# Performance work log

Measured on AMD Instinct MI355X. Metric: run time of the kernel, lower is better.

## Reference

```python
import jax, jax.numpy as jnp
import numpy as np

K = 10      # neighbors; conv width math 10 -> 3 -> 1
EPS = 1e-5  # InstanceNorm2d default eps (affine=False)
NEG = 0.2   # leaky relu slope


def _instnorm(x):
    m = x.mean(axis=(2, 3), keepdims=True)
    v = x.var(axis=(2, 3), keepdims=True)  # biased var, as in torch instance_norm
    return (x - m) * jax.lax.rsqrt(v + EPS)


def _conv13(x, w, b, s):
    y = jax.lax.conv_general_dilated(x, w, (1, s), 'VALID',
                                     dimension_numbers=('NCHW', 'OIHW', 'NCHW'))
    return y + b[None, :, None, None]


def _block(x, wA, bA, wB, bB):
    # Sequential(conv(1,3,stride(1,3)), IN, ReLU, conv(1,3), IN, ReLU)
    y = jax.nn.relu(_instnorm(_conv13(x, wA, bA, 3)))
    return jax.nn.relu(_instnorm(_conv13(y, wB, bB, 1)))


def _knn_idx(coords, k):
    # coords [B,2,N] -> k nearest neighbor indices [B,N,k] (self excluded)
    pts = coords.transpose(0, 2, 1)
    sq = (pts ** 2).sum(-1)
    dist = sq[:, :, None] + sq[:, None, :] - 2.0 * jnp.einsum('bnc,bmc->bnm', pts, pts)
    dist = jnp.clip(dist, 1e-12)
    _, idx = jax.lax.top_k(-dist, k + 1)  # smallest distances, sorted
    return idx[:, :, 1:]


def _gather_nb(x, idx):
    # x [B,C,N], idx [B,N,k] -> [B,C,N,k]
    return jax.vmap(lambda f, i: f[:, i])(x, idx)


def _graph_feat(feats, idx):
    nb = _gather_nb(feats, idx)
    ctr = jnp.broadcast_to(feats[..., None], nb.shape)
    return jnp.concatenate([ctr, nb - ctr], axis=1)  # [B,2C,N,k]


def _cos_angle(coords, idx):
    nei = _gather_nb(coords, idx)          # [B,2,N,k]
    ctr = coords[..., None]                # [B,2,N,1]
    dot = (ctr * nei).sum(axis=1, keepdims=True)
    na = jnp.sqrt((ctr ** 2).sum(axis=1, keepdims=True))
    nb = jnp.sqrt((nei ** 2).sum(axis=1, keepdims=True))
    return dot / (na * nb)                 # [B,1,N,k]


def _c1(w, x):
    # 1x1 conv, no bias
    return jnp.einsum('oi,bihw->bohw', w, x)


def _forward(coords, features, W1, W2, W3, W3o, a1wA, a1bA, a1wB, a1bB,
             a2wA, a2bA, a2wB, a2bB, angwA, angbA, angwB, angbB):
    B, C, N = features.shape
    lrelu = lambda x: jax.nn.leaky_relu(x, NEG)
    x0 = features[..., None]
    # KNN depends only on coords: all three torch graph builds give identical indices
    idx = _knn_idx(coords, K)
    x1_old = _graph_feat(features, idx)                         # [B,2C,N,K]
    x1 = _block(x1_old, a1wA, a1bA, a1wB, a1bB)                 # [B,C,N,1]
    # angle_enc1 is shared and idx identical -> f_ang1 == f_ang2
    f_ang = _block(_cos_angle(coords, idx), angwA, angbA, angwB, angbB)
    x2 = _block(_graph_feat(x1[..., 0], idx), a2wA, a2bA, a2wB, a2bB)
    x3 = jnp.concatenate([x0, x1 + f_ang, x2 + f_ang], axis=1)  # [B,3C,N,1]
    x3 = lrelu(_instnorm(_c1(W3, x3))).reshape(B, -1, N)
    x1o = lrelu(_instnorm(_c1(W1, x1_old))).max(axis=-1, keepdims=True)   # [B,C,N,1]
    x2o = lrelu(_instnorm(_c1(W2, _graph_feat(x1o[..., 0], idx)))).max(axis=-1, keepdims=True)
    x3o = jnp.concatenate([x0, x1o, x2o], axis=1)               # [B,4C,N,1]
    x3o = lrelu(_instnorm(_c1(W3o, x3o))).reshape(B, -1, N)
    return x3 + x3o


def setup_inputs():
    key = jax.random.key(0)
    ks = jax.random.split(key, 20)
    B, C, N = 4, 128, 4096
    r = lambda i, shp, sc=1.0: jax.random.normal(ks[i], shp, jnp.float32) * sc
    s = 0.05
    return {
        'coords': r(0, (B, 2, N)),
        'features': r(1, (B, C, N)),
        'W1': r(2, (C, 2 * C), s),
        'W2': r(3, (2 * C, 2 * C), s),
        'W3': r(4, (C, 3 * C), s),
        'W3o': r(5, (C, 4 * C), s),
        'a1wA': r(6, (C, 2 * C, 1, 3), s), 'a1bA': r(7, (C,), s),
        'a1wB': r(8, (C, C, 1, 3), s), 'a1bB': r(9, (C,), s),
        'a2wA': r(10, (C, 2 * C, 1, 3), s), 'a2bA': r(11, (C,), s),
        'a2wB': r(12, (C, C, 1, 3), s), 'a2bB': r(13, (C,), s),
        'angwA': r(14, (C, 1, 1, 3), s), 'angbA': r(15, (C,), s),
        'angwB': r(16, (C, C, 1, 3), s), 'angbB': r(17, (C,), s),
    }


def reference(coords, features, W1, W2, W3, W3o, a1wA, a1bA, a1wB, a1bB,
              a2wA, a2bA, a2wB, a2bB, angwA, angbA, angwB, angbB):
    return _forward(coords, features, W1, W2, W3, W3o, a1wA, a1bA, a1wB, a1bB,
                    a2wA, a2bA, a2wB, a2bB, angwA, angbA, angwB, angbB)
```

## Files before the change

### kernel.cpp

```cpp
#include <hip/hip_runtime.h>
#include <hip/hip_bf16.h>

typedef unsigned long long ull;

#define BN 4
#define CH 128
#define NP 4096
#define KNB 10
#define EPSI 1e-5f
#define GM_PTS 16
#define CA_PTS 16

#define FMA4(A, W, F) do { (A).x += (W).x*(F); (A).y += (W).y*(F); \
                           (A).z += (W).z*(F); (A).w += (W).w*(F); } while(0)

__device__ __forceinline__ ull shfl_xor_u64(ull v, int mask) {
    unsigned lo = (unsigned)(v & 0xFFFFFFFFu);
    unsigned hi = (unsigned)(v >> 32);
    lo = __shfl_xor(lo, mask);
    hi = __shfl_xor(hi, mask);
    return ((ull)hi << 32) | lo;
}

__device__ __forceinline__ int clampj(int j) { return ((unsigned)j < (unsigned)NP) ? j : 0; }

__device__ __forceinline__ unsigned short f2bf(float f) {
    unsigned u = __float_as_uint(f);
    unsigned r = u + 0x7FFFu + ((u >> 16) & 1u);
    return (unsigned short)(r >> 16);
}
__device__ __forceinline__ float bf2f(unsigned short h) {
    return __uint_as_float(((unsigned)h) << 16);
}
__device__ __forceinline__ float4 bfload4(const unsigned short* p) {
    ushort4 h = *(const ushort4*)p;
    float4 r; r.x = bf2f(h.x); r.y = bf2f(h.y); r.z = bf2f(h.z); r.w = bf2f(h.w);
    return r;
}

__device__ __forceinline__ void d_packA(const float* w, float* WT, int i) {
    int co = i % CH, ci = (i / CH) % CH, s = i / (CH * CH);
    float val;
    if (s == 0) {
        val = 0.f;
        for (int dk = 0; dk < 3; dk++)
            val += w[(co * 256 + ci) * 3 + dk] - w[(co * 256 + 128 + ci) * 3 + dk];
    } else {
        val = w[(co * 256 + 128 + ci) * 3 + (s - 1)];
    }
    WT[i] = val;
}
__device__ __forceinline__ void d_packB(const float* w, float* WT, int i) {
    int co = i % CH, ci = (i / CH) % CH, dk = i / (CH * CH);
    WT[i] = w[(co * CH + ci) * 3 + dk];
}
__device__ __forceinline__ void d_packUV(const float* w, float* Wu, float* Wn, int Cout, int i) {
    int co = i % Cout, ci = i / Cout;
    float a = w[co * 256 + ci], bb = w[co * 256 + 128 + ci];
    Wu[i] = a - bb; Wn[i] = bb;
}
__device__ __forceinline__ void d_packP(const float* w, float* WT, int Cin, int Cout, int i) {
    int co = i % Cout, ci = i / Cout;
    WT[i] = w[co * Cin + ci];
}

__global__ void pack_all(const float* __restrict__ a1wA, const float* __restrict__ a2wA,
                         const float* __restrict__ a1wB, const float* __restrict__ a2wB,
                         const float* __restrict__ angwB, const float* __restrict__ W1,
                         const float* __restrict__ W2, const float* __restrict__ W3,
                         const float* __restrict__ W3o, const float* __restrict__ angwA,
                         float* __restrict__ WA1T, float* __restrict__ WA2T,
                         float* __restrict__ WB1T, float* __restrict__ WB2T,
                         float* __restrict__ WBAT,
                         float* __restrict__ W1U, float* __restrict__ W1N,
                         float* __restrict__ W2U, float* __restrict__ W2N,
                         float* __restrict__ W3T, float* __restrict__ W3OT,
                         float* __restrict__ WANGA) {
    int i = blockIdx.x * 256 + threadIdx.x;
    const int sA = 4 * CH * CH;
    const int sB = 3 * CH * CH;
    if (i < sA) { d_packA(a1wA, WA1T, i); return; } i -= sA;
    if (i < sA) { d_packA(a2wA, WA2T, i); return; } i -= sA;
    if (i < sB) { d_packB(a1wB, WB1T, i); return; } i -= sB;
    if (i < sB) { d_packB(a2wB, WB2T, i); return; } i -= sB;
    if (i < sB) { d_packB(angwB, WBAT, i); return; } i -= sB;
    if (i < CH * CH) { d_packUV(W1, W1U, W1N, CH, i); return; } i -= CH * CH;
    if (i < CH * 256) { d_packUV(W2, W2U, W2N, 256, i); return; } i -= CH * 256;
    if (i < 384 * CH) { d_packP(W3, W3T, 384, CH, i); return; } i -= 384 * CH;
    if (i < 512 * CH) { d_packP(W3o, W3OT, 512, CH, i); return; } i -= 512 * CH;
    if (i < 3 * CH) { d_packP(angwA, WANGA, 3, CH, i); return; }
}

__global__ void ftrans_kernel(const float* __restrict__ feats, float* __restrict__ F) {
    int i = blockIdx.x * 256 + threadIdx.x;
    if (i >= BN * CH * NP) return;
    int n = i % NP, c = (i / NP) % CH, b = i / (NP * CH);
    F[(b * NP + n) * CH + c] = feats[i];
}

__global__ void knn_kernel(const float* __restrict__ coords, int* __restrict__ IDX) {
    int gw = blockIdx.x * 4 + (threadIdx.x >> 6);
    int b = gw / NP;
    int n = gw % NP;
    int lane = threadIdx.x & 63;
    float xn = coords[(b * 2 + 0) * NP + n];
    float yn = coords[(b * 2 + 1) * NP + n];
    float sn = __fadd_rn(__fmul_rn(xn, xn), __fmul_rn(yn, yn));
    ull a[11];
    #pragma unroll
    for (int q = 0; q < 11; q++) a[q] = 0xFFFFFFFFFFFFFFFFULL;
    for (int m = lane; m < NP; m += 64) {
        float xm = coords[(b * 2 + 0) * NP + m];
        float ym = coords[(b * 2 + 1) * NP + m];
        float sm = __fadd_rn(__fmul_rn(xm, xm), __fmul_rn(ym, ym));
        float dot = __fmaf_rn(yn, ym, __fmul_rn(xn, xm));
        float d = __fsub_rn(__fadd_rn(sn, sm), __fmul_rn(2.0f, dot));
        d = fmaxf(d, 1e-12f);
        ull key = ((ull)__float_as_uint(d) << 32) | (unsigned)m;
        if (key < a[10]) {
            a[10] = key;
            #pragma unroll
            for (int q = 10; q > 0; --q)
                if (a[q] < a[q - 1]) { ull t = a[q]; a[q] = a[q - 1]; a[q - 1] = t; }
        }
    }
    for (int r = 0; r < 11; ++r) {
        ull k = a[0];
        ull mk = k;
        #pragma unroll
        for (int off = 1; off < 64; off <<= 1) {
            ull o = shfl_xor_u64(mk, off);
            mk = (o < mk) ? o : mk;
        }
        if (k == mk) {
            #pragma unroll
            for (int q = 0; q < 10; ++q) a[q] = a[q + 1];
            a[10] = 0xFFFFFFFFFFFFFFFFULL;
        }
        if (lane == 0 && r > 0) IDX[(b * NP + n) * KNB + (r - 1)] = (int)(mk & 0xFFFFFFFFu);
    }
}

__global__ void cosangle_kernel(const float* __restrict__ coords, const int* __restrict__ IDX,
                                float* __restrict__ COSA) {
    int i = blockIdx.x * 256 + threadIdx.x;
    if (i >= BN * NP * KNB) return;
    int n = (i / KNB) % NP, b = i / (KNB * NP);
    int j = clampj(IDX[i]);
    float xc = coords[(b * 2 + 0) * NP + n], yc = coords[(b * 2 + 1) * NP + n];
    float xm = coords[(b * 2 + 0) * NP + j], ym = coords[(b * 2 + 1) * NP + j];
    float dot = xc * xm + yc * ym;
    float na = sqrtf(xc * xc + yc * yc);
    float nb2 = sqrtf(xm * xm + ym * ym);
    COSA[i] = dot / fmaxf(na * nb2, 1e-30f);
}

__global__ __launch_bounds__(256) void convA_kernel(const float* __restrict__ Fin,
                             const int* __restrict__ IDX,
                             const float* __restrict__ WT, float* __restrict__ YA,
                             float* __restrict__ PART,
                             const float* __restrict__ STATS, int slot) {
    __shared__ __align__(16) float ctr[CA_PTS][CH];
    __shared__ __align__(16) unsigned short nbh[CA_PTS][9][CH];
    __shared__ int jidx[CA_PTS * 9];
    int b = blockIdx.x / (NP / CA_PTS);
    int chunk = blockIdx.x % (NP / CA_PTS);
    int n0 = chunk * CA_PTS;
    int cog = threadIdx.x & 31;
    int pg  = threadIdx.x >> 5;
    const float* SB = (slot >= 0) ? &STATS[((size_t)(slot * BN + b) * 256) * 2] : nullptr;
    if (threadIdx.x < CA_PTS * 9) {
        int n = threadIdx.x / 9, kk = threadIdx.x % 9;
        jidx[threadIdx.x] = clampj(IDX[(b * NP + n0 + n) * KNB + kk]);
    }
    __syncthreads();
    for (int v4 = threadIdx.x; v4 < CA_PTS * 32; v4 += 256) {
        int n = v4 >> 5, c4 = v4 & 31;
        float4 x = *(const float4*)&Fin[(size_t)(b * NP + n0 + n) * CH + c4 * 4];
        if (SB) {
            float4 s0 = *(const float4*)&SB[c4 * 8];
            float4 s1 = *(const float4*)&SB[c4 * 8 + 4];
            x.x = fmaxf((x.x - s0.x) * s0.y, 0.f);
            x.y = fmaxf((x.y - s0.z) * s0.w, 0.f);
            x.z = fmaxf((x.z - s1.x) * s1.y, 0.f);
            x.w = fmaxf((x.w - s1.z) * s1.w, 0.f);
        }
        *(float4*)&ctr[n][c4 * 4] = x;
    }
    for (int v4 = threadIdx.x; v4 < CA_PTS * 9 * 32; v4 += 256) {
        int n = v4 / 288, rem = v4 % 288, kk = rem >> 5, c4 = rem & 31;
        float4 x = *(const float4*)&Fin[(size_t)(b * NP + jidx[n * 9 + kk]) * CH + c4 * 4];
        if (SB) {
            float4 s0 = *(const float4*)&SB[c4 * 8];
            float4 s1 = *(const float4*)&SB[c4 * 8 + 4];
            x.x = fmaxf((x.x - s0.x) * s0.y, 0.f);
            x.y = fmaxf((x.y - s0.z) * s0.w, 0.f);
            x.z = fmaxf((x.z - s1.x) * s1.y, 0.f);
            x.w = fmaxf((x.w - s1.z) * s1.w, 0.f);
        }
        ushort4 h;
        h.x = f2bf(x.x); h.y = f2bf(x.y); h.z = f2bf(x.z); h.w = f2bf(x.w);
        *(ushort4*)&nbh[n][kk][c4 * 4] = h;
    }
    __syncthreads();
    const float4* W4 = (const float4*)WT;
    const int p0 = pg * 2, p1 = pg * 2 + 1;
    float4 cacc0, cacc1;
    cacc0.x = cacc0.y = cacc0.z = cacc0.w = 0.f;
    cacc1 = cacc0;
    for (int ci = 0; ci < CH; ci += 4) {
        float4 xa = *(const float4*)&ctr[p0][ci];
        float4 xb = *(const float4*)&ctr[p1][ci];
        #pragma unroll
        for (int u = 0; u < 4; ++u) {
            float4 w = W4[(ci + u) * 32 + cog];
            float fa = ((const float*)&xa)[u];
            float fb = ((const float*)&xb)[u];
            FMA4(cacc0, w, fa); FMA4(cacc1, w, fb);
        }
    }
    float4 t00 = cacc0, t01 = cacc0, t02 = cacc0;
    float4 t10 = cacc1, t11 = cacc1, t12 = cacc1;
    for (int dk = 0; dk < 3; ++dk) {
        const float4* Wd = W4 + (size_t)(1 + dk) * (CH * 32);
        const unsigned short* a00 = &nbh[p0][0 * 3 + dk][0];
        const unsigned short* a01 = &nbh[p0][1 * 3 + dk][0];
        const unsigned short* a02 = &nbh[p0][2 * 3 + dk][0];
        const unsigned short* a10 = &nbh[p1][0 * 3 + dk][0];
        const unsigned short* a11 = &nbh[p1][1 * 3 + dk][0];
        const unsigned short* a12 = &nbh[p1][2 * 3 + dk][0];
        for (int ci = 0; ci < CH; ci += 4) {
            float4 x00 = bfload4(&a00[ci]);
            float4 x01 = bfload4(&a01[ci]);
            float4 x02 = bfload4(&a02[ci]);
            float4 x10 = bfload4(&a10[ci]);
            float4 x11 = bfload4(&a11[ci]);
            float4 x12 = bfload4(&a12[ci]);
            #pragma unroll
            for (int u = 0; u < 4; ++u) {
                float4 w = Wd[(ci + u) * 32 + cog];
                FMA4(t00, w, ((const float*)&x00)[u]);
                FMA4(t01, w, ((const float*)&x01)[u]);
                FMA4(t02, w, ((const float*)&x02)[u]);
                FMA4(t10, w, ((const float*)&x10)[u]);
                FMA4(t11, w, ((const float*)&x11)[u]);
                FMA4(t12, w, ((const float*)&x12)[u]);
            }
        }
    }
    {
        size_t base0 = ((size_t)(b * NP + n0 + p0) * 3) * CH + cog * 4;
        *(float4*)&YA[base0 + 0 * CH] = t00;
        *(float4*)&YA[base0 + 1 * CH] = t01;
        *(float4*)&YA[base0 + 2 * CH] = t02;
        size_t base1 = ((size_t)(b * NP + n0 + p1) * 3) * CH + cog * 4;
        *(float4*)&YA[base1 + 0 * CH] = t10;
        *(float4*)&YA[base1 + 1 * CH] = t11;
        *(float4*)&YA[base1 + 2 * CH] = t12;
    }
    float s4[4], q4[4];
    s4[0] = t00.x + t01.x + t02.x + t10.x + t11.x + t12.x;
    s4[1] = t00.y + t01.y + t02.y + t10.y + t11.y + t12.y;
    s4[2] = t00.z + t01.z + t02.z + t10.z + t11.z + t12.z;
    s4[3] = t00.w + t01.w + t02.w + t10.w + t11.w + t12.w;
    q4[0] = t00.x*t00.x + t01.x*t01.x + t02.x*t02.x + t10.x*t10.x + t11.x*t11.x + t12.x*t12.x;
    q4[1] = t00.y*t00.y + t01.y*t01.y + t02.y*t02.y + t10.y*t10.y + t11.y*t11.y + t12.y*t12.y;
    q4[2] = t00.z*t00.z + t01.z*t01.z + t02.z*t02.z + t10.z*t10.z + t11.z*t11.z + t12.z*t12.z;
    q4[3] = t00.w*t00.w + t01.w*t01.w + t02.w*t02.w + t10.w*t10.w + t11.w*t11.w + t12.w*t12.w;
    __syncthreads();
    float* red = (float*)&nbh[0][0][0];
    #pragma unroll
    for (int j = 0; j < 4; ++j) {
        red[((pg * 32 + cog) * 4 + j) * 2 + 0] = s4[j];
        red[((pg * 32 + cog) * 4 + j) * 2 + 1] = q4[j];
    }
    __syncthreads();
    if (threadIdx.x < CH) {
        int c = threadIdx.x;
        float ss = 0.f, qq = 0.f;
        #pragma unroll
        for (int g = 0; g < 8; ++g) {
            ss += red[((g * 32 + (c >> 2)) * 4 + (c & 3)) * 2 + 0];
            qq += red[((g * 32 + (c >> 2)) * 4 + (c & 3)) * 2 + 1];
        }
        PART[((size_t)(b * (NP / CA_PTS) + chunk) * 256 + c) * 2 + 0] = ss;
        PART[((size_t)(b * (NP / CA_PTS) + chunk) * 256 + c) * 2 + 1] = qq;
    }
}

__global__ void angA_kernel(const float* __restrict__ COSA, const float* __restrict__ WT,
                            float* __restrict__ YA, float* __restrict__ PART) {
    __shared__ float ca[32][10];
    int b = blockIdx.x / (NP / 32);
    int chunk = blockIdx.x % (NP / 32);
    int n0 = chunk * 32;
    int co = threadIdx.x;
    for (int v = threadIdx.x; v < 320; v += 128) {
        int nn = v / 10, kk = v % 10;
        ca[nn][kk] = COSA[(b * NP + n0 + nn) * KNB + kk];
    }
    float w0 = WT[co], w1 = WT[CH + co], w2 = WT[2 * CH + co];
    __syncthreads();
    float sum = 0.f, sq = 0.f;
    for (int nn = 0; nn < 32; nn++) {
        #pragma unroll
        for (int t = 0; t < 3; t++) {
            float v = w0 * ca[nn][3 * t] + w1 * ca[nn][3 * t + 1] + w2 * ca[nn][3 * t + 2];
            YA[((b * NP + n0 + nn) * 3 + t) * CH + co] = v;
            sum += v; sq += v * v;
        }
    }
    PART[((b * (NP / 32) + chunk) * 256 + co) * 2 + 0] = sum;
    PART[((b * (NP / 32) + chunk) * 256 + co) * 2 + 1] = sq;
}

template <int CIN, int NCOG>
__device__ __forceinline__ void gemm_16pt(const float* lds, const float* __restrict__ WT,
                                          int cog, int pg, float4 acc[4]) {
    const float4* W4 = (const float4*)WT;
    const float* xb = lds + pg * 4 * CIN;
    for (int ci = 0; ci < CIN; ci += 4) {
        float4 x0 = *(const float4*)&xb[0 * CIN + ci];
        float4 x1 = *(const float4*)&xb[1 * CIN + ci];
        float4 x2 = *(const float4*)&xb[2 * CIN + ci];
        float4 x3 = *(const float4*)&xb[3 * CIN + ci];
        #pragma unroll
        for (int u = 0; u < 4; ++u) {
            float4 w = W4[(ci + u) * NCOG + cog];
            float f0 = ((const float*)&x0)[u];
            float f1 = ((const float*)&x1)[u];
            float f2 = ((const float*)&x2)[u];
            float f3 = ((const float*)&x3)[u];
            FMA4(acc[0], w, f0); FMA4(acc[1], w, f1);
            FMA4(acc[2], w, f2); FMA4(acc[3], w, f3);
        }
    }
}

template <int NCOG>
__device__ __forceinline__ void reduce_stats(const float* s4, const float* q4,
                                             float* red, float* __restrict__ PART,
                                             int b, int chunk, int nchunks,
                                             int pg, int cog) {
    constexpr int COUT = NCOG * 4;
    __syncthreads();
    #pragma unroll
    for (int j = 0; j < 4; ++j) {
        red[((pg * NCOG + cog) * 4 + j) * 2 + 0] = s4[j];
        red[((pg * NCOG + cog) * 4 + j) * 2 + 1] = q4[j];
    }
    __syncthreads();
    int c = threadIdx.x;
    if (c < COUT) {
        float ss = 0.f, qq = 0.f;
        #pragma unroll
        for (int g = 0; g < 4; ++g) {
            ss += red[((g * NCOG + (c >> 2)) * 4 + (c & 3)) * 2 + 0];
            qq += red[((g * NCOG + (c >> 2)) * 4 + (c & 3)) * 2 + 1];
        }
        PART[((size_t)(b * nchunks + chunk) * 256 + c) * 2 + 0] = ss;
        PART[((size_t)(b * nchunks + chunk) * 256 + c) * 2 + 1] = qq;
    }
}

template <int NCOG>
__device__ __forceinline__ void out16(const float4 acc[4], float* __restrict__ OUT,
                                      int b, int n0, int pg, int cog,
                                      float s4[4], float q4[4]) {
    constexpr int COUT = NCOG * 4;
    #pragma unroll
    for (int p = 0; p < 4; ++p) {
        *(float4*)&OUT[(size_t)(b * NP + n0 + pg * 4 + p) * COUT + cog * 4] = acc[p];
        s4[0] += acc[p].x; s4[1] += acc[p].y; s4[2] += acc[p].z; s4[3] += acc[p].w;
        q4[0] += acc[p].x * acc[p].x; q4[1] += acc[p].y * acc[p].y;
        q4[2] += acc[p].z * acc[p].z; q4[3] += acc[p].w * acc[p].w;
    }
}

template <int CIN, int NCOG>
__global__ void pixel_gemm_t(const float* __restrict__ IN_, const float* __restrict__ WT,
                             float* __restrict__ OUT, const float* __restrict__ STATS,
                             int slot, int act, float* __restrict__ PART) {
    constexpr int COUT = NCOG * 4;
    constexpr int BD = 4 * NCOG;
    __shared__ __align__(16) float ldsin[16 * CIN];
    int b = blockIdx.x / (NP / 16);
    int chunk = blockIdx.x % (NP / 16);
    int n0 = chunk * 16;
    int cog = threadIdx.x & (NCOG - 1);
    int pg = threadIdx.x / NCOG;
    constexpr int nv4 = 16 * CIN / 4;
    if (slot >= 0) {
        int cbase = (4 * threadIdx.x) & 127;
        const float* st = &STATS[((slot * BN + b) * 256 + cbase) * 2];
        float m0 = st[0], r0 = st[1], m1 = st[2], r1 = st[3];
        float m2 = st[4], r2 = st[5], m3 = st[6], r3 = st[7];
        for (int v4 = threadIdx.x; v4 < nv4; v4 += BD) {
            float4 x = *(const float4*)&IN_[(size_t)(b * NP + n0) * CIN + 4 * v4];
            float v0 = (x.x - m0) * r0, v1 = (x.y - m1) * r1;
            float v2 = (x.z - m2) * r2, v3 = (x.w - m3) * r3;
            if (act) {
                x.x = (v0 >= 0.f) ? v0 : 0.2f * v0;
                x.y = (v1 >= 0.f) ? v1 : 0.2f * v1;
                x.z = (v2 >= 0.f) ? v2 : 0.2f * v2;
                x.w = (v3 >= 0.f) ? v3 : 0.2f * v3;
            } else {
                x.x = fmaxf(v0, 0.f); x.y = fmaxf(v1, 0.f);
                x.z = fmaxf(v2, 0.f); x.w = fmaxf(v3, 0.f);
            }
            *(float4*)&ldsin[4 * v4] = x;
        }
    } else {
        for (int v4 = threadIdx.x; v4 < nv4; v4 += BD)
            *(float4*)&ldsin[4 * v4] =
                *(const float4*)&IN_[(size_t)(b * NP + n0) * CIN + 4 * v4];
    }
    __syncthreads();
    float4 acc[4];
    #pragma unroll
    for (int p = 0; p < 4; ++p) acc[p].x = acc[p].y = acc[p].z = acc[p].w = 0.f;
    gemm_16pt<CIN, NCOG>(ldsin, WT, cog, pg, acc);
    float s4[4] = {0,0,0,0}, q4[4] = {0,0,0,0};
    out16<NCOG>(acc, OUT, b, n0, pg, cog, s4, q4);
    if (PART)
        reduce_stats<NCOG>(s4, q4, ldsin, PART, b, chunk, NP / 16, pg, cog);
}

__global__ void stats_final(const float* __restrict__ PART, float* __restrict__ STATS,
                            int S, int Cc, int slot, int nch) {
    __shared__ float ssum[256], ssq[256];
    int bc = blockIdx.x;
    int b = bc / Cc, c = bc % Cc;
    float sum = 0.f, sq = 0.f;
    for (int ch = threadIdx.x; ch < nch; ch += 256) {
        sum += PART[((b * nch + ch) * 256 + c) * 2 + 0];
        sq  += PART[((b * nch + ch) * 256 + c) * 2 + 1];
    }
    ssum[threadIdx.x] = sum; ssq[threadIdx.x] = sq;
    __syncthreads();
    for (int s = 128; s > 0; s >>= 1) {
        if (threadIdx.x < s) {
            ssum[threadIdx.x] += ssum[threadIdx.x + s];
            ssq[threadIdx.x]  += ssq[threadIdx.x + s];
        }
        __syncthreads();
    }
    if (threadIdx.x == 0) {
        float mean = ssum[0] / (float)S;
        float var = fmaxf(ssq[0] / (float)S - mean * mean, 0.f);
        STATS[((slot * BN + b) * 256 + c) * 2 + 0] = mean;
        STATS[((slot * BN + b) * 256 + c) * 2 + 1] = rsqrtf(var + EPSI);
    }
}

template <int NCOG>
__global__ void gathermax_t(const float* __restrict__ X, const float* __restrict__ Wu,
                            const float* __restrict__ V, const int* __restrict__ IDX,
                            float* __restrict__ M, float* __restrict__ PART,
                            const float* __restrict__ STATS, int slot) {
    constexpr int COUT = NCOG * 4;
    __shared__ __align__(16) float rows[GM_PTS * CH];
    int b = blockIdx.x / (NP / GM_PTS);
    int chunk = blockIdx.x % (NP / GM_PTS);
    int n0 = chunk * GM_PTS;
    int cog = threadIdx.x & (NCOG - 1);
    int pg = threadIdx.x / NCOG;
    if (slot >= 0) {
        int c0 = (4 * threadIdx.x) & 127;
        const float* st = &STATS[((slot * BN + b) * 256 + c0) * 2];
        float m0 = st[0], r0 = st[1], m1 = st[2], r1 = st[3];
        float m2 = st[4], r2 = st[5], m3 = st[6], r3 = st[7];
        for (int v4 = threadIdx.x; v4 < GM_PTS * CH / 4; v4 += COUT) {
            float4 x = *(const float4*)&X[(size_t)(b * NP + n0) * CH + v4 * 4];
            float v0 = (x.x - m0) * r0, v1 = (x.y - m1) * r1;
            float v2 = (x.z - m2) * r2, v3 = (x.w - m3) * r3;
            x.x = (v0 >= 0.f) ? v0 : 0.2f * v0;
            x.y = (v1 >= 0.f) ? v1 : 0.2f * v1;
            x.z = (v2 >= 0.f) ? v2 : 0.2f * v2;
            x.w = (v3 >= 0.f) ? v3 : 0.2f * v3;
            *(float4*)&rows[v4 * 4] = x;
        }
    } else {
        for (int v4 = threadIdx.x; v4 < GM_PTS * CH / 4; v4 += COUT)
            *(float4*)&rows[v4 * 4] = *(const float4*)&X[(size_t)(b * NP + n0) * CH + v4 * 4];
    }
    __syncthreads();
    float4 acc[4];
    #pragma unroll
    for (int p = 0; p < 4; ++p) acc[p].x = acc[p].y = acc[p].z = acc[p].w = 0.f;
    gemm_16pt<CH, NCOG>(rows, Wu, cog, pg, acc);
    float s4[4] = {0,0,0,0}, q4[4] = {0,0,0,0};
    #pragma unroll
    for (int p = 0; p < 4; ++p) {
        int nn = n0 + pg * 4 + p;
        float4 u = acc[p];
        float4 best; best.x = best.y = best.z = best.w = -3.4e38f;
        for (int k = 0; k < KNB; ++k) {
            int j = clampj(IDX[(b * NP + nn) * KNB + k]);
            float4 vv = *(const float4*)&V[(size_t)(b * NP + j) * COUT + cog * 4];
            vv.x += u.x; vv.y += u.y; vv.z += u.z; vv.w += u.w;
            s4[0] += vv.x; s4[1] += vv.y; s4[2] += vv.z; s4[3] += vv.w;
            q4[0] += vv.x * vv.x; q4[1] += vv.y * vv.y;
            q4[2] += vv.z * vv.z; q4[3] += vv.w * vv.w;
            best.x = fmaxf(best.x, vv.x); best.y = fmaxf(best.y, vv.y);
            best.z = fmaxf(best.z, vv.z); best.w = fmaxf(best.w, vv.w);
        }
        *(float4*)&M[(size_t)(b * NP + nn) * COUT + cog * 4] = best;
    }
    __syncthreads();
    reduce_stats<NCOG>(s4, q4, rows, PART, b, chunk, NP / GM_PTS, pg, cog);
}

__global__ void head3_kernel(const float* __restrict__ F, const float* __restrict__ X1,
                             const float* __restrict__ X2, const float* __restrict__ FANG,
                             const float* __restrict__ WT, float* __restrict__ Y3,
                             float* __restrict__ PART, const float* __restrict__ STATS) {
    __shared__ __align__(16) float lds[16 * 384];
    int b = blockIdx.x / (NP / 16);
    int chunk = blockIdx.x % (NP / 16);
    int n0 = chunk * 16;
    int cog = threadIdx.x & 31;
    int pg = threadIdx.x >> 5;
    const float* S1 = &STATS[((size_t)(1 * BN + b) * 256) * 2];
    const float* S5 = &STATS[((size_t)(5 * BN + b) * 256) * 2];
    const float* S3 = &STATS[((size_t)(3 * BN + b) * 256) * 2];
    for (int v4 = threadIdx.x; v4 < 16 * 96; v4 += 128) {
        int nn = v4 / 96, q4 = v4 % 96;
        int part = q4 >> 5, c4 = q4 & 31;
        size_t base = (size_t)(b * NP + n0 + nn) * CH + c4 * 4;
        float4 val;
        if (part == 0) val = *(const float4*)&F[base];
        else {
            const float* src = (part == 1) ? X1 : X2;
            const float* SX = (part == 1) ? S1 : S5;
            float4 xx = *(const float4*)&src[base];
            float4 aa = *(const float4*)&FANG[base];
            float4 sx0 = *(const float4*)&SX[c4 * 8];
            float4 sx1 = *(const float4*)&SX[c4 * 8 + 4];
            float4 sa0 = *(const float4*)&S3[c4 * 8];
            float4 sa1 = *(const float4*)&S3[c4 * 8 + 4];
            val.x = fmaxf((xx.x - sx0.x) * sx0.y, 0.f) + fmaxf((aa.x - sa0.x) * sa0.y, 0.f);
            val.y = fmaxf((xx.y - sx0.z) * sx0.w, 0.f) + fmaxf((aa.y - sa0.z) * sa0.w, 0.f);
            val.z = fmaxf((xx.z - sx1.x) * sx1.y, 0.f) + fmaxf((aa.z - sa1.x) * sa1.y, 0.f);
            val.w = fmaxf((xx.w - sx1.z) * sx1.w, 0.f) + fmaxf((aa.w - sa1.z) * sa1.w, 0.f);
        }
        *(float4*)&lds[v4 * 4] = val;
    }
    __syncthreads();
    float4 acc[4];
    #pragma unroll
    for (int p = 0; p < 4; ++p) acc[p].x = acc[p].y = acc[p].z = acc[p].w = 0.f;
    gemm_16pt<384, 32>(lds, WT, cog, pg, acc);
    float s4[4] = {0,0,0,0}, q4[4] = {0,0,0,0};
    out16<32>(acc, Y3, b, n0, pg, cog, s4, q4);
    reduce_stats<32>(s4, q4, lds, PART, b, chunk, NP / 16, pg, cog);
}

__global__ void head3o_kernel(const float* __restrict__ F, const float* __restrict__ X1O,
                              const float* __restrict__ X2O, const float* __restrict__ WT,
                              float* __restrict__ Y3O, float* __restrict__ PART,
                              const float* __restrict__ STATS) {
    __shared__ __align__(16) float lds[16 * 512];
    int b = blockIdx.x / (NP / 16);
    int chunk = blockIdx.x % (NP / 16);
    int n0 = chunk * 16;
    int cog = threadIdx.x & 31;
    int pg = threadIdx.x >> 5;
    const float* S6 = &STATS[((size_t)(6 * BN + b) * 256) * 2];
    const float* S7 = &STATS[((size_t)(7 * BN + b) * 256) * 2];
    for (int v4 = threadIdx.x; v4 < 16 * 128; v4 += 128) {
        int nn = v4 >> 7, q4 = v4 & 127;
        float4 val;
        if (q4 < 32) {
            val = *(const float4*)&F[(size_t)(b * NP + n0 + nn) * CH + q4 * 4];
        } else if (q4 < 64) {
            int c4 = q4 - 32;
            float4 x = *(const float4*)&X1O[(size_t)(b * NP + n0 + nn) * CH + c4 * 4];
            float4 s0 = *(const float4*)&S6[c4 * 8];
            float4 s1 = *(const float4*)&S6[c4 * 8 + 4];
            float v0 = (x.x - s0.x) * s0.y, v1 = (x.y - s0.z) * s0.w;
            float v2 = (x.z - s1.x) * s1.y, v3 = (x.w - s1.z) * s1.w;
            val.x = (v0 >= 0.f) ? v0 : 0.2f * v0;
            val.y = (v1 >= 0.f) ? v1 : 0.2f * v1;
            val.z = (v2 >= 0.f) ? v2 : 0.2f * v2;
            val.w = (v3 >= 0.f) ? v3 : 0.2f * v3;
        } else {
            int c4 = q4 - 64;
            float4 x = *(const float4*)&X2O[(size_t)(b * NP + n0 + nn) * 256 + c4 * 4];
            float4 s0 = *(const float4*)&S7[c4 * 8];
            float4 s1 = *(const float4*)&S7[c4 * 8 + 4];
            float v0 = (x.x - s0.x) * s0.y, v1 = (x.y - s0.z) * s0.w;
            float v2 = (x.z - s1.x) * s1.y, v3 = (x.w - s1.z) * s1.w;
            val.x = (v0 >= 0.f) ? v0 : 0.2f * v0;
            val.y = (v1 >= 0.f) ? v1 : 0.2f * v1;
            val.z = (v2 >= 0.f) ? v2 : 0.2f * v2;
            val.w = (v3 >= 0.f) ? v3 : 0.2f * v3;
        }
        *(float4*)&lds[v4 * 4] = val;
    }
    __syncthreads();
    float4 acc[4];
    #pragma unroll
    for (int p = 0; p < 4; ++p) acc[p].x = acc[p].y = acc[p].z = acc[p].w = 0.f;
    gemm_16pt<512, 32>(lds, WT, cog, pg, acc);
    float s4[4] = {0,0,0,0}, q4[4] = {0,0,0,0};
    out16<32>(acc, Y3O, b, n0, pg, cog, s4, q4);
    reduce_stats<32>(s4, q4, lds, PART, b, chunk, NP / 16, pg, cog);
}

__global__ void final_kernel(const float* __restrict__ Y3, const float* __restrict__ Y3O,
                             const float* __restrict__ STATS, float* __restrict__ out) {
    __shared__ float T[64][129];
    int b = blockIdx.x / (NP / 64);
    int n0 = (blockIdx.x % (NP / 64)) * 64;
    int co = threadIdx.x;
    float m3 = STATS[((8 * BN + b) * 256 + co) * 2 + 0];
    float r3 = STATS[((8 * BN + b) * 256 + co) * 2 + 1];
    float m3o = STATS[((9 * BN + b) * 256 + co) * 2 + 0];
    float r3o = STATS[((9 * BN + b) * 256 + co) * 2 + 1];
    for (int j = 0; j < 64; j++) {
        size_t idx = (size_t)(b * NP + n0 + j) * CH + co;
        float v3 = (Y3[idx] - m3) * r3;
        v3 = (v3 >= 0.f) ? v3 : 0.2f * v3;
        float v3o = (Y3O[idx] - m3o) * r3o;
        v3o = (v3o >= 0.f) ? v3o : 0.2f * v3o;
        T[j][co] = v3 + v3o;
    }
    __syncthreads();
    for (int rr = 0; rr < 64; rr++) {
        int r = rr * 2 + (threadIdx.x >> 6);
        int j = threadIdx.x & 63;
        out[(size_t)(b * CH + r) * NP + n0 + j] = T[j][r];
    }
}

extern "C" void kernel_launch(void* const* d_in, const int* in_sizes, int n_in,
                              void* d_out, int out_size, void* d_ws, size_t ws_size,
                              hipStream_t stream) {
    const float* coords   = (const float*)d_in[0];
    const float* features = (const float*)d_in[1];
    const float* W1   = (const float*)d_in[2];
    const float* W2   = (const float*)d_in[3];
    const float* W3   = (const float*)d_in[4];
    const float* W3o  = (const float*)d_in[5];
    const float* a1wA = (const float*)d_in[6];
    const float* a1wB = (const float*)d_in[8];
    const float* a2wA = (const float*)d_in[10];
    const float* a2wB = (const float*)d_in[12];
    const float* angwA = (const float*)d_in[14];
    const float* angwB = (const float*)d_in[16];
    float* out = (float*)d_out;
    float* ws = (float*)d_ws;
    (void)ws_size; (void)in_sizes; (void)n_in; (void)out_size;

    size_t off = 0;
    float* WA1T  = ws + off; off += 4 * CH * CH;
    float* WA2T  = ws + off; off += 4 * CH * CH;
    float* WB1T  = ws + off; off += 3 * CH * CH;
    float* WB2T  = ws + off; off += 3 * CH * CH;
    float* WBAT  = ws + off; off += 3 * CH * CH;
    float* WANGA = ws + off; off += 512;
    float* W1U   = ws + off; off += CH * CH;
    float* W1N   = ws + off; off += CH * CH;
    float* W2U   = ws + off; off += CH * 256;
    float* W2N   = ws + off; off += CH * 256;
    float* W3T   = ws + off; off += 384 * CH;
    float* W3OT  = ws + off; off += 512 * CH;
    int*   IDX   = (int*)(ws + off); off += (size_t)BN * NP * KNB;
    float* COSA  = ws + off; off += (size_t)BN * NP * KNB;
    float* PART  = ws + off; off += (size_t)BN * 1024 * 256 * 2;
    float* STATS = ws + off; off += 10 * BN * 256 * 2;
    const size_t UNIT = (size_t)BN * NP * CH;
    float* POOL  = ws + off; off += 7 * UNIT;

    float* F    = POOL + 0 * UNIT;
    float* YA   = POOL + 1 * UNIT;
    float* X1   = POOL + 4 * UNIT;
    float* FANG = POOL + 5 * UNIT;
    float* X2   = POOL + 6 * UNIT;
    float* Y3   = POOL + 1 * UNIT;
    float* V1   = POOL + 2 * UNIT;
    float* M1   = POOL + 6 * UNIT;
    float* V2   = POOL + 4 * UNIT;
    float* M2   = POOL + 2 * UNIT;
    float* Y3O  = POOL + 4 * UNIT;

    pack_all<<<1730, 256, 0, stream>>>(a1wA, a2wA, a1wB, a2wB, angwB, W1, W2, W3, W3o, angwA,
                                       WA1T, WA2T, WB1T, WB2T, WBAT,
                                       W1U, W1N, W2U, W2N, W3T, W3OT, WANGA);

    ftrans_kernel<<<(BN * CH * NP + 255) / 256, 256, 0, stream>>>(features, F);
    knn_kernel<<<BN * NP / 4, 256, 0, stream>>>(coords, IDX);
    cosangle_kernel<<<(BN * NP * KNB + 255) / 256, 256, 0, stream>>>(coords, IDX, COSA);

    auto sfin = [&](int S, int Cc, int slot, int nch) {
        stats_final<<<BN * Cc, 256, 0, stream>>>(PART, STATS, S, Cc, slot, nch);
    };

    convA_kernel<<<BN * (NP / CA_PTS), 256, 0, stream>>>(F, IDX, WA1T, YA, PART, STATS, -1);
    sfin(3 * NP, CH, 0, NP / CA_PTS);
    pixel_gemm_t<384, 32><<<BN * (NP / 16), 128, 0, stream>>>(YA, WB1T, X1, STATS, 0, 0, PART);
    sfin(NP, CH, 1, NP / 16);

    angA_kernel<<<BN * (NP / 32), 128, 0, stream>>>(COSA, WANGA, YA, PART);
    sfin(3 * NP, CH, 2, NP / 32);
    pixel_gemm_t<384, 32><<<BN * (NP / 16), 128, 0, stream>>>(YA, WBAT, FANG, STATS, 2, 0, PART);
    sfin(NP, CH, 3, NP / 16);

    convA_kernel<<<BN * (NP / CA_PTS), 256, 0, stream>>>(X1, IDX, WA2T, YA, PART, STATS, 1);
    sfin(3 * NP, CH, 4, NP / CA_PTS);
    pixel_gemm_t<384, 32><<<BN * (NP / 16), 128, 0, stream>>>(YA, WB2T, X2, STATS, 4, 0, PART);
    sfin(NP, CH, 5, NP / 16);

    head3_kernel<<<BN * (NP / 16), 128, 0, stream>>>(F, X1, X2, FANG, W3T, Y3, PART, STATS);
    sfin(NP, CH, 8, NP / 16);

    pixel_gemm_t<128, 32><<<BN * (NP / 16), 128, 0, stream>>>(F, W1N, V1, STATS, -1, 0, nullptr);
    gathermax_t<32><<<BN * (NP / GM_PTS), 128, 0, stream>>>(F, W1U, V1, IDX, M1, PART, STATS, -1);
    sfin(NP * KNB, CH, 6, NP / GM_PTS);

    pixel_gemm_t<128, 64><<<BN * (NP / 16), 256, 0, stream>>>(M1, W2N, V2, STATS, 6, 1, nullptr);
    gathermax_t<64><<<BN * (NP / GM_PTS), 256, 0, stream>>>(M1, W2U, V2, IDX, M2, PART, STATS, 6);
    sfin(NP * KNB, 256, 7, NP / GM_PTS);

    head3o_kernel<<<BN * (NP / 16), 128, 0, stream>>>(F, M1, M2, W3OT, Y3O, PART, STATS);
    sfin(NP, CH, 9, NP / 16);
    final_kernel<<<BN * (NP / 64), 128, 0, stream>>>(Y3, Y3O, STATS, out);
}
```

Measured before the change: 841.7 us.

## Double points per block in pixel GEMMs and stage inputs as bf16 in LDS

The per-point GEMM kernels (pixel_gemm_t, head3, head3o) now process 32 points per block instead of 16, with each thread holding 8 point accumulators. Each weight float4 loaded from global memory is therefore reused across twice as many points. Inputs are staged in shared memory as bf16, which keeps the LDS footprint the same and halves LDS read traffic. The trade-offs are bf16 rounding of activations, which costs accuracy, more registers per thread, and half as many blocks. The stats partial counts are updated to match.

```diff
diff --git a/kernel.cpp b/kernel.cpp
--- a/kernel.cpp
+++ b/kernel.cpp
@@ -36,6 +36,10 @@
     ushort4 h = *(const ushort4*)p;
     float4 r; r.x = bf2f(h.x); r.y = bf2f(h.y); r.z = bf2f(h.z); r.w = bf2f(h.w);
     return r;
+}
+__device__ __forceinline__ ushort4 bf4(float4 x) {
+    ushort4 h; h.x = f2bf(x.x); h.y = f2bf(x.y); h.z = f2bf(x.z); h.w = f2bf(x.w);
+    return h;
 }
 
 __device__ __forceinline__ void d_packA(const float* w, float* WT, int i) {
@@ -198,9 +202,7 @@
             x.z = fmaxf((x.z - s1.x) * s1.y, 0.f);
             x.w = fmaxf((x.w - s1.z) * s1.w, 0.f);
         }
-        ushort4 h;
-        h.x = f2bf(x.x); h.y = f2bf(x.y); h.z = f2bf(x.z); h.w = f2bf(x.w);
-        *(ushort4*)&nbh[n][kk][c4 * 4] = h;
+        *(ushort4*)&nbh[n][kk][c4 * 4] = bf4(x);
     }
     __syncthreads();
     const float4* W4 = (const float4*)WT;
@@ -337,6 +339,36 @@
     }
 }
 
+template <int CIN, int NCOG>
+__device__ __forceinline__ void gemm_32pt(const unsigned short* lds,
+                                          const float* __restrict__ WT,
+                                          int cog, int pg, float4 acc[8]) {
+    const float4* W4 = (const float4*)WT;
+    const unsigned short* xb = lds + pg * 8 * CIN;
+    for (int ci = 0; ci < CIN; ci += 4) {
+        float4 x0 = bfload4(&xb[0 * CIN + ci]);
+        float4 x1 = bfload4(&xb[1 * CIN + ci]);
+        float4 x2 = bfload4(&xb[2 * CIN + ci]);
+        float4 x3 = bfload4(&xb[3 * CIN + ci]);
+        float4 x4 = bfload4(&xb[4 * CIN + ci]);
+        float4 x5 = bfload4(&xb[5 * CIN + ci]);
+        float4 x6 = bfload4(&xb[6 * CIN + ci]);
+        float4 x7 = bfload4(&xb[7 * CIN + ci]);
+        #pragma unroll
+        for (int u = 0; u < 4; ++u) {
+            float4 w = W4[(ci + u) * NCOG + cog];
+            FMA4(acc[0], w, ((const float*)&x0)[u]);
+            FMA4(acc[1], w, ((const float*)&x1)[u]);
+            FMA4(acc[2], w, ((const float*)&x2)[u]);
+            FMA4(acc[3], w, ((const float*)&x3)[u]);
+            FMA4(acc[4], w, ((const float*)&x4)[u]);
+            FMA4(acc[5], w, ((const float*)&x5)[u]);
+            FMA4(acc[6], w, ((const float*)&x6)[u]);
+            FMA4(acc[7], w, ((const float*)&x7)[u]);
+        }
+    }
+}
+
 template <int NCOG>
 __device__ __forceinline__ void reduce_stats(const float* s4, const float* q4,
                                              float* red, float* __restrict__ PART,
@@ -364,13 +396,13 @@
 }
 
 template <int NCOG>
-__device__ __forceinline__ void out16(const float4 acc[4], float* __restrict__ OUT,
+__device__ __forceinline__ void out32(const float4 acc[8], float* __restrict__ OUT,
                                       int b, int n0, int pg, int cog,
                                       float s4[4], float q4[4]) {
     constexpr int COUT = NCOG * 4;
     #pragma unroll
-    for (int p = 0; p < 4; ++p) {
-        *(float4*)&OUT[(size_t)(b * NP + n0 + pg * 4 + p) * COUT + cog * 4] = acc[p];
+    for (int p = 0; p < 8; ++p) {
+        *(float4*)&OUT[(size_t)(b * NP + n0 + pg * 8 + p) * COUT + cog * 4] = acc[p];
         s4[0] += acc[p].x; s4[1] += acc[p].y; s4[2] += acc[p].z; s4[3] += acc[p].w;
         q4[0] += acc[p].x * acc[p].x; q4[1] += acc[p].y * acc[p].y;
         q4[2] += acc[p].z * acc[p].z; q4[3] += acc[p].w * acc[p].w;
@@ -383,13 +415,13 @@
                              int slot, int act, float* __restrict__ PART) {
     constexpr int COUT = NCOG * 4;
     constexpr int BD = 4 * NCOG;
-    __shared__ __align__(16) float ldsin[16 * CIN];
-    int b = blockIdx.x / (NP / 16);
-    int chunk = blockIdx.x % (NP / 16);
-    int n0 = chunk * 16;
+    __shared__ __align__(16) unsigned short ldsin[32 * CIN];
+    int b = blockIdx.x / (NP / 32);
+    int chunk = blockIdx.x % (NP / 32);
+    int n0 = chunk * 32;
     int cog = threadIdx.x & (NCOG - 1);
     int pg = threadIdx.x / NCOG;
-    constexpr int nv4 = 16 * CIN / 4;
+    constexpr int nv4 = 32 * CIN / 4;
     if (slot >= 0) {
         int cbase = (4 * threadIdx.x) & 127;
         const float* st = &STATS[((slot * BN + b) * 256 + cbase) * 2];
@@ -408,22 +440,23 @@
                 x.x = fmaxf(v0, 0.f); x.y = fmaxf(v1, 0.f);
                 x.z = fmaxf(v2, 0.f); x.w = fmaxf(v3, 0.f);
             }
-            *(float4*)&ldsin[4 * v4] = x;
+            *(ushort4*)&ldsin[4 * v4] = bf4(x);
         }
     } else {
-        for (int v4 = threadIdx.x; v4 < nv4; v4 += BD)
-            *(float4*)&ldsin[4 * v4] =
-                *(const float4*)&IN_[(size_t)(b * NP + n0) * CIN + 4 * v4];
-    }
-    __syncthreads();
-    float4 acc[4];
-    #pragma unroll
-    for (int p = 0; p < 4; ++p) acc[p].x = acc[p].y = acc[p].z = acc[p].w = 0.f;
-    gemm_16pt<CIN, NCOG>(ldsin, WT, cog, pg, acc);
+        for (int v4 = threadIdx.x; v4 < nv4; v4 += BD) {
+            float4 x = *(const float4*)&IN_[(size_t)(b * NP + n0) * CIN + 4 * v4];
+            *(ushort4*)&ldsin[4 * v4] = bf4(x);
+        }
+    }
+    __syncthreads();
+    float4 acc[8];
+    #pragma unroll
+    for (int p = 0; p < 8; ++p) acc[p].x = acc[p].y = acc[p].z = acc[p].w = 0.f;
+    gemm_32pt<CIN, NCOG>(ldsin, WT, cog, pg, acc);
     float s4[4] = {0,0,0,0}, q4[4] = {0,0,0,0};
-    out16<NCOG>(acc, OUT, b, n0, pg, cog, s4, q4);
+    out32<NCOG>(acc, OUT, b, n0, pg, cog, s4, q4);
     if (PART)
-        reduce_stats<NCOG>(s4, q4, ldsin, PART, b, chunk, NP / 16, pg, cog);
+        reduce_stats<NCOG>(s4, q4, (float*)ldsin, PART, b, chunk, NP / 32, pg, cog);
 }
 
 __global__ void stats_final(const float* __restrict__ PART, float* __restrict__ STATS,
@@ -515,16 +548,16 @@
                              const float* __restrict__ X2, const float* __restrict__ FANG,
                              const float* __restrict__ WT, float* __restrict__ Y3,
                              float* __restrict__ PART, const float* __restrict__ STATS) {
-    __shared__ __align__(16) float lds[16 * 384];
-    int b = blockIdx.x / (NP / 16);
-    int chunk = blockIdx.x % (NP / 16);
-    int n0 = chunk * 16;
+    __shared__ __align__(16) unsigned short lds[32 * 384];
+    int b = blockIdx.x / (NP / 32);
+    int chunk = blockIdx.x % (NP / 32);
+    int n0 = chunk * 32;
     int cog = threadIdx.x & 31;
     int pg = threadIdx.x >> 5;
     const float* S1 = &STATS[((size_t)(1 * BN + b) * 256) * 2];
     const float* S5 = &STATS[((size_t)(5 * BN + b) * 256) * 2];
     const float* S3 = &STATS[((size_t)(3 * BN + b) * 256) * 2];
-    for (int v4 = threadIdx.x; v4 < 16 * 96; v4 += 128) {
+    for (int v4 = threadIdx.x; v4 < 32 * 96; v4 += 128) {
         int nn = v4 / 96, q4 = v4 % 96;
         int part = q4 >> 5, c4 = q4 & 31;
         size_t base = (size_t)(b * NP + n0 + nn) * CH + c4 * 4;
@@ -544,31 +577,31 @@
             val.z = fmaxf((xx.z - sx1.x) * sx1.y, 0.f) + fmaxf((aa.z - sa1.x) * sa1.y, 0.f);
             val.w = fmaxf((xx.w - sx1.z) * sx1.w, 0.f) + fmaxf((aa.w - sa1.z) * sa1.w, 0.f);
         }
-        *(float4*)&lds[v4 * 4] = val;
-    }
-    __syncthreads();
-    float4 acc[4];
-    #pragma unroll
-    for (int p = 0; p < 4; ++p) acc[p].x = acc[p].y = acc[p].z = acc[p].w = 0.f;
-    gemm_16pt<384, 32>(lds, WT, cog, pg, acc);
+        *(ushort4*)&lds[v4 * 4] = bf4(val);
+    }
+    __syncthreads();
+    float4 acc[8];
+    #pragma unroll
+    for (int p = 0; p < 8; ++p) acc[p].x = acc[p].y = acc[p].z = acc[p].w = 0.f;
+    gemm_32pt<384, 32>(lds, WT, cog, pg, acc);
     float s4[4] = {0,0,0,0}, q4[4] = {0,0,0,0};
-    out16<32>(acc, Y3, b, n0, pg, cog, s4, q4);
-    reduce_stats<32>(s4, q4, lds, PART, b, chunk, NP / 16, pg, cog);
+    out32<32>(acc, Y3, b, n0, pg, cog, s4, q4);
+    reduce_stats<32>(s4, q4, (float*)lds, PART, b, chunk, NP / 32, pg, cog);
 }
 
 __global__ void head3o_kernel(const float* __restrict__ F, const float* __restrict__ X1O,
                               const float* __restrict__ X2O, const float* __restrict__ WT,
                               float* __restrict__ Y3O, float* __restrict__ PART,
                               const float* __restrict__ STATS) {
-    __shared__ __align__(16) float lds[16 * 512];
-    int b = blockIdx.x / (NP / 16);
-    int chunk = blockIdx.x % (NP / 16);
-    int n0 = chunk * 16;
+    __shared__ __align__(16) unsigned short lds[32 * 512];
+    int b = blockIdx.x / (NP / 32);
+    int chunk = blockIdx.x % (NP / 32);
+    int n0 = chunk * 32;
     int cog = threadIdx.x & 31;
     int pg = threadIdx.x >> 5;
     const float* S6 = &STATS[((size_t)(6 * BN + b) * 256) * 2];
     const float* S7 = &STATS[((size_t)(7 * BN + b) * 256) * 2];
-    for (int v4 = threadIdx.x; v4 < 16 * 128; v4 += 128) {
+    for (int v4 = threadIdx.x; v4 < 32 * 128; v4 += 128) {
         int nn = v4 >> 7, q4 = v4 & 127;
         float4 val;
         if (q4 < 32) {
@@ -596,16 +629,16 @@
             val.z = (v2 >= 0.f) ? v2 : 0.2f * v2;
             val.w = (v3 >= 0.f) ? v3 : 0.2f * v3;
         }
-        *(float4*)&lds[v4 * 4] = val;
-    }
-    __syncthreads();
-    float4 acc[4];
-    #pragma unroll
-    for (int p = 0; p < 4; ++p) acc[p].x = acc[p].y = acc[p].z = acc[p].w = 0.f;
-    gemm_16pt<512, 32>(lds, WT, cog, pg, acc);
+        *(ushort4*)&lds[v4 * 4] = bf4(val);
+    }
+    __syncthreads();
+    float4 acc[8];
+    #pragma unroll
+    for (int p = 0; p < 8; ++p) acc[p].x = acc[p].y = acc[p].z = acc[p].w = 0.f;
+    gemm_32pt<512, 32>(lds, WT, cog, pg, acc);
     float s4[4] = {0,0,0,0}, q4[4] = {0,0,0,0};
-    out16<32>(acc, Y3O, b, n0, pg, cog, s4, q4);
-    reduce_stats<32>(s4, q4, lds, PART, b, chunk, NP / 16, pg, cog);
+    out32<32>(acc, Y3O, b, n0, pg, cog, s4, q4);
+    reduce_stats<32>(s4, q4, (float*)lds, PART, b, chunk, NP / 32, pg, cog);
 }
 
 __global__ void final_kernel(const float* __restrict__ Y3, const float* __restrict__ Y3O,
@@ -699,31 +732,31 @@
 
     convA_kernel<<<BN * (NP / CA_PTS), 256, 0, stream>>>(F, IDX, WA1T, YA, PART, STATS, -1);
     sfin(3 * NP, CH, 0, NP / CA_PTS);
-    pixel_gemm_t<384, 32><<<BN * (NP / 16), 128, 0, stream>>>(YA, WB1T, X1, STATS, 0, 0, PART);
-    sfin(NP, CH, 1, NP / 16);
+    pixel_gemm_t<384, 32><<<BN * (NP / 32), 128, 0, stream>>>(YA, WB1T, X1, STATS, 0, 0, PART);
+    sfin(NP, CH, 1, NP / 32);
 
     angA_kernel<<<BN * (NP / 32), 128, 0, stream>>>(COSA, WANGA, YA, PART);
     sfin(3 * NP, CH, 2, NP / 32);
-    pixel_gemm_t<384, 32><<<BN * (NP / 16), 128, 0, stream>>>(YA, WBAT, FANG, STATS, 2, 0, PART);
-    sfin(NP, CH, 3, NP / 16);
+    pixel_gemm_t<384, 32><<<BN * (NP / 32), 128, 0, stream>>>(YA, WBAT, FANG, STATS, 2, 0, PART);
+    sfin(NP, CH, 3, NP / 32);
 
     convA_kernel<<<BN * (NP / CA_PTS), 256, 0, stream>>>(X1, IDX, WA2T, YA, PART, STATS, 1);
     sfin(3 * NP, CH, 4, NP / CA_PTS);
-    pixel_gemm_t<384, 32><<<BN * (NP / 16), 128, 0, stream>>>(YA, WB2T, X2, STATS, 4, 0, PART);
-    sfin(NP, CH, 5, NP / 16);
-
-    head3_kernel<<<BN * (NP / 16), 128, 0, stream>>>(F, X1, X2, FANG, W3T, Y3, PART, STATS);
-    sfin(NP, CH, 8, NP / 16);
-
-    pixel_gemm_t<128, 32><<<BN * (NP / 16), 128, 0, stream>>>(F, W1N, V1, STATS, -1, 0, nullptr);
+    pixel_gemm_t<384, 32><<<BN * (NP / 32), 128, 0, stream>>>(YA, WB2T, X2, STATS, 4, 0, PART);
+    sfin(NP, CH, 5, NP / 32);
+
+    head3_kernel<<<BN * (NP / 32), 128, 0, stream>>>(F, X1, X2, FANG, W3T, Y3, PART, STATS);
+    sfin(NP, CH, 8, NP / 32);
+
+    pixel_gemm_t<128, 32><<<BN * (NP / 32), 128, 0, stream>>>(F, W1N, V1, STATS, -1, 0, nullptr);
     gathermax_t<32><<<BN * (NP / GM_PTS), 128, 0, stream>>>(F, W1U, V1, IDX, M1, PART, STATS, -1);
     sfin(NP * KNB, CH, 6, NP / GM_PTS);
 
-    pixel_gemm_t<128, 64><<<BN * (NP / 16), 256, 0, stream>>>(M1, W2N, V2, STATS, 6, 1, nullptr);
+    pixel_gemm_t<128, 64><<<BN * (NP / 32), 256, 0, stream>>>(M1, W2N, V2, STATS, 6, 1, nullptr);
     gathermax_t<64><<<BN * (NP / GM_PTS), 256, 0, stream>>>(M1, W2U, V2, IDX, M2, PART, STATS, 6);
     sfin(NP * KNB, 256, 7, NP / GM_PTS);
 
-    head3o_kernel<<<BN * (NP / 16), 128, 0, stream>>>(F, M1, M2, W3OT, Y3O, PART, STATS);
-    sfin(NP, CH, 9, NP / 16);
+    head3o_kernel<<<BN * (NP / 32), 128, 0, stream>>>(F, M1, M2, W3OT, Y3O, PART, STATS);
+    sfin(NP, CH, 9, NP / 32);
     final_kernel<<<BN * (NP / 64), 128, 0, stream>>>(Y3, Y3O, STATS, out);
 }
```

Measured after the change: 1.104 ms. +31.2%, slower.
